# Performance work log

Measured on AMD Instinct MI355X. Metric: run time of the kernel, lower is better.

The kernel has to match this reference:

```python
import jax, jax.numpy as jnp
import numpy as np

N = 100000      # nodes
E = 3200000     # directed edges (avg degree 32)
D_IN = 128
H = 64
NEG_INF = -1e30


def setup_inputs() -> dict:
    key = jax.random.key(0)
    ks = jax.random.split(key, 16)
    s = 0.05
    return {
        "x": jax.random.normal(ks[0], (N, D_IN), jnp.float32),
        "edge_index": jax.random.randint(ks[1], (2, E), 0, N, jnp.int32),
        "ready": jax.random.randint(ks[2], (N, 1), 0, 2, jnp.int32),
        "W1": jax.random.normal(ks[3], (D_IN, H), jnp.float32) * s,
        "b1": jnp.zeros((H,), jnp.float32),
        "W2": jax.random.normal(ks[4], (H, H), jnp.float32) * s,
        "b2": jnp.zeros((H,), jnp.float32),
        "W3": jax.random.normal(ks[5], (H, H), jnp.float32) * s,
        "b3": jnp.zeros((H,), jnp.float32),
        "W4": jax.random.normal(ks[6], (H, H), jnp.float32) * s,
        "b4": jnp.zeros((H,), jnp.float32),
        "W5": jax.random.normal(ks[7], (H, 1), jnp.float32) * s,
        "b5": jnp.zeros((1,), jnp.float32),
        "Wdn": jax.random.normal(ks[8], (H, 1), jnp.float32) * s,
        "bdn": jnp.zeros((1,), jnp.float32),
        "Wv": jax.random.normal(ks[9], (H, 1), jnp.float32) * s,
        "bv": jnp.zeros((1,), jnp.float32),
    }


def _gcn_norm(edge_index):
    # add self-loops, then symmetric normalization.
    # flow='target_to_source': aggregate at row=edge_index[0], gather from col=edge_index[1],
    # degree computed on the row index (PyG gcn_norm with flow='target_to_source').
    loops = jnp.arange(N, dtype=edge_index.dtype)
    row = jnp.concatenate([edge_index[0], loops])
    col = jnp.concatenate([edge_index[1], loops])
    deg = jax.ops.segment_sum(jnp.ones(row.shape[0], jnp.float32), row, num_segments=N)
    dinv = jnp.where(deg > 0, jax.lax.rsqrt(deg), 0.0)
    norm = dinv[row] * dinv[col]
    return row, col, norm


def _gcn_conv(x, W, b, row, col, norm):
    h = x @ W                               # [N, d_out]
    m = norm[:, None] * h[col]              # gather messages from col
    out = jax.ops.segment_sum(m, row, num_segments=N)  # scatter-add at row
    return out + b


def reference(x, edge_index, ready, W1, b1, W2, b2, W3, b3, W4, b4, W5, b5, Wdn, bdn, Wv, bv):
    row, col, norm = _gcn_norm(edge_index)
    h = jax.nn.relu(_gcn_conv(x, W1, b1, row, col, norm))
    h = jax.nn.relu(_gcn_conv(h, W2, b2, row, col, norm))
    h = jax.nn.relu(_gcn_conv(h, W3, b3, row, col, norm))
    h = jax.nn.relu(_gcn_conv(h, W4, b4, row, col, norm))
    probs_nodes = _gcn_conv(h, W5, b5, row, col, norm)[:, 0]   # [N]
    x_mean = jnp.mean(h, axis=0)                               # [H]
    v = x_mean @ Wv + bv                                       # [1]
    prob_nothing = x_mean @ Wdn + bdn                          # [1]
    logits = jnp.concatenate([probs_nodes, prob_nothing])      # [N+1]
    mask = jnp.concatenate([ready[:, 0].astype(bool), jnp.array([True])])
    # masked softmax: softmax restricted to ready nodes + 'do nothing' slot;
    # non-ready positions get probability 0 (fixed-shape equivalent of torch's
    # boolean-index + softmax over the selected entries).
    probs = jax.nn.softmax(jnp.where(mask, logits, NEG_INF))
    return probs, v
```

## Files before the change

kernel.cpp:

```cpp
#include <hip/hip_runtime.h>
#include <hip/hip_bf16.h>
#include <hip/hip_fp16.h>


#define WAVE 64
#define BSHIFT 9
#define BROWS 512
#define ACHUNK 8192
#define CAP 17408

using half8  = __attribute__((ext_vector_type(8))) _Float16;
using float4v = __attribute__((ext_vector_type(4))) float;

__device__ __forceinline__ float waveSum(float v) {
  #pragma unroll
  for (int o = 32; o; o >>= 1) v += __shfl_xor(v, o);
  return v;
}
__device__ __forceinline__ float waveMax(float v) {
  #pragma unroll
  for (int o = 32; o; o >>= 1) v = fmaxf(v, __shfl_xor(v, o));
  return v;
}

__global__ void bucket_init(int* __restrict__ bucket_fill, int nbkt) {
  int b = blockIdx.x * blockDim.x + threadIdx.x;
  if (b < nbkt) bucket_fill[b] = b * CAP;
}

__global__ __launch_bounds__(256) void bin_edges(const int* __restrict__ ei,
                                                 int* __restrict__ bucket_fill,
                                                 int* __restrict__ eb, int E) {
  __shared__ int hist[256], basee[256], rank[256];
  int t = threadIdx.x;
  hist[t] = 0; rank[t] = 0;
  __syncthreads();
  int c0 = blockIdx.x * ACHUNK;
  #pragma unroll
  for (int k = 0; k < ACHUNK / 256; ++k) {
    int e = c0 + k * 256 + t;
    if (e < E) atomicAdd(&hist[ei[e] >> BSHIFT], 1);
  }
  __syncthreads();
  if (hist[t]) basee[t] = atomicAdd(&bucket_fill[t], hist[t]);
  __syncthreads();
  #pragma unroll
  for (int k = 0; k < ACHUNK / 256; ++k) {
    int e = c0 + k * 256 + t;
    if (e < E) {
      int r = ei[e], c = ei[E + e];
      int bb = r >> BSHIFT;
      int p = basee[bb] + atomicAdd(&rank[bb], 1);
      eb[p] = ((r & (BROWS - 1)) << 17) | c;
    }
  }
}

__global__ __launch_bounds__(256) void csr_bucket(const int* __restrict__ eb,
                                                  const int* __restrict__ bucket_fill,
                                                  int* __restrict__ row_s,
                                                  int* __restrict__ row_e,
                                                  float* __restrict__ dinv,
                                                  int* __restrict__ col_s, int N) {
  __shared__ int deg[BROWS], locp[BROWS], fill[BROWS], sh[256];
  int b = blockIdx.x;
  int base = b << BSHIFT;
  int R = min(BROWS, N - base);
  int t = threadIdx.x;
  deg[t] = 0; deg[t + 256] = 0;
  fill[t] = 0; fill[t + 256] = 0;
  __syncthreads();
  int E0 = b * CAP, E1 = bucket_fill[b];
  for (int e = E0 + t; e < E1; e += 256) atomicAdd(&deg[eb[e] >> 17], 1);
  __syncthreads();
  int d0 = deg[2 * t], d1 = deg[2 * t + 1];
  int s = d0 + d1;
  sh[t] = s;
  __syncthreads();
  for (int o = 1; o < 256; o <<= 1) {
    int x = (t >= o) ? sh[t - o] : 0;
    __syncthreads();
    sh[t] += x;
    __syncthreads();
  }
  int ex = sh[t] - s;
  locp[2 * t] = ex;
  locp[2 * t + 1] = ex + d0;
  __syncthreads();
  for (int i = t; i < R; i += 256) {
    int st = E0 + locp[i];
    row_s[base + i] = st;
    row_e[base + i] = st + deg[i];
    dinv[base + i] = rsqrtf((float)(deg[i] + 1));
  }
  for (int e = E0 + t; e < E1; e += 256) {
    int v = eb[e];
    int li = v >> 17;
    int p = E0 + locp[li] + atomicAdd(&fill[li], 1);
    col_s[p] = v & 0x1FFFF;
  }
}

template <int K, bool A32>
__global__ __launch_bounds__(256) void gemm_f16(const void* __restrict__ Ain,
                                                const float* __restrict__ Wg,
                                                const float* __restrict__ dinv,
                                                __half* __restrict__ Y, int N) {
  __shared__ _Float16 Wt[64][K + 8];
  int t = threadIdx.x;
  for (int idx = t; idx < K * 64; idx += 256) {
    int k = idx >> 6, n = idx & 63;
    Wt[n][k] = (_Float16)Wg[idx];
  }
  __syncthreads();
  int wave = t >> 6, lane = t & 63;
  int m = lane & 15, quad = lane >> 4;
  int r0 = blockIdx.x * 64 + wave * 16;
  float4v acc0 = {0.f, 0.f, 0.f, 0.f}, acc1 = {0.f, 0.f, 0.f, 0.f};
  float4v acc2 = {0.f, 0.f, 0.f, 0.f}, acc3 = {0.f, 0.f, 0.f, 0.f};
  int gr = r0 + m;
  bool valid = gr < N;
  int grs = valid ? gr : 0;
  const half8* arow = (const half8*)((const _Float16*)Ain + (size_t)grs * K);
  const float4* arow32 = (const float4*)((const float*)Ain + (size_t)grs * K);
  #pragma unroll
  for (int k0 = 0; k0 < K; k0 += 32) {
    half8 a = {};
    if (valid) {
      if (A32) {
        float4 f0 = arow32[(k0 >> 2) + quad * 2];
        float4 f1 = arow32[(k0 >> 2) + quad * 2 + 1];
        a = half8{(_Float16)f0.x, (_Float16)f0.y, (_Float16)f0.z, (_Float16)f0.w,
                  (_Float16)f1.x, (_Float16)f1.y, (_Float16)f1.z, (_Float16)f1.w};
      } else {
        a = arow[(k0 >> 3) + quad];
      }
    }
    half8 b0 = *(const half8*)&Wt[ 0 + m][k0 + quad * 8];
    half8 b1 = *(const half8*)&Wt[16 + m][k0 + quad * 8];
    half8 b2 = *(const half8*)&Wt[32 + m][k0 + quad * 8];
    half8 b3 = *(const half8*)&Wt[48 + m][k0 + quad * 8];
    acc0 = __builtin_amdgcn_mfma_f32_16x16x32_f16(a, b0, acc0, 0, 0, 0);
    acc1 = __builtin_amdgcn_mfma_f32_16x16x32_f16(a, b1, acc1, 0, 0, 0);
    acc2 = __builtin_amdgcn_mfma_f32_16x16x32_f16(a, b2, acc2, 0, 0, 0);
    acc3 = __builtin_amdgcn_mfma_f32_16x16x32_f16(a, b3, acc3, 0, 0, 0);
  }
  #pragma unroll
  for (int r = 0; r < 4; ++r) {
    int row = r0 + quad * 4 + r;
    if (row < N) {
      float dv = dinv[row];
      __half* dst = Y + (size_t)row * 64;
      dst[ 0 + m] = __float2half(acc0[r] * dv);
      dst[16 + m] = __float2half(acc1[r] * dv);
      dst[32 + m] = __float2half(acc2[r] * dv);
      dst[48 + m] = __float2half(acc3[r] * dv);
    }
  }
}

__device__ __forceinline__ float2 gather_row(const __half2* __restrict__ Y2,
                                             const int* __restrict__ col_s,
                                             int i, int p0, int p1,
                                             int lane, int half, int ch2) {
  float2 a0 = {0.f, 0.f}, a1 = {0.f, 0.f};
  if (half == 0) a0 = __half22float2(Y2[(size_t)i * 32 + ch2]);
  for (int base = p0; base < p1; base += 64) {
    int m = min(64, p1 - base);
    int c = 0;
    if (lane < m) c = col_s[base + lane];
    int j = 0;
    for (; j + 8 <= m; j += 8) {
      int c0 = __shfl(c, j + half);
      int c1 = __shfl(c, j + 2 + half);
      int c2 = __shfl(c, j + 4 + half);
      int c3 = __shfl(c, j + 6 + half);
      float2 y0 = __half22float2(Y2[(size_t)c0 * 32 + ch2]);
      float2 y1 = __half22float2(Y2[(size_t)c1 * 32 + ch2]);
      float2 y2 = __half22float2(Y2[(size_t)c2 * 32 + ch2]);
      float2 y3 = __half22float2(Y2[(size_t)c3 * 32 + ch2]);
      a0.x += y0.x + y1.x; a0.y += y0.y + y1.y;
      a1.x += y2.x + y3.x; a1.y += y2.y + y3.y;
    }
    for (; j < m; j += 2) {
      int idx = j + half;
      int cc = __shfl(c, idx);
      if (idx < m) {
        float2 y = __half22float2(Y2[(size_t)cc * 32 + ch2]);
        a0.x += y.x; a0.y += y.y;
      }
    }
  }
  float2 s;
  s.x = a0.x + a1.x;
  s.y = a0.y + a1.y;
  s.x += __shfl_xor(s.x, 32);
  s.y += __shfl_xor(s.y, 32);
  return s;
}

__global__ __launch_bounds__(256) void agg64(const __half* __restrict__ Ys,
                                             const int* __restrict__ col_s,
                                             const int* __restrict__ row_s,
                                             const int* __restrict__ row_e,
                                             const float* __restrict__ dinv,
                                             const float* __restrict__ bias,
                                             __half* __restrict__ Xh, int N) {
  int i = blockIdx.x * 4 + (threadIdx.x >> 6);
  if (i >= N) return;
  int lane = threadIdx.x & 63;
  int half = lane >> 5, ch2 = lane & 31;
  const __half2* Y2 = (const __half2*)Ys;
  float2 s = gather_row(Y2, col_s, i, row_s[i], row_e[i], lane, half, ch2);
  if (half == 0) {
    float2 b2 = ((const float2*)bias)[ch2];
    float di = dinv[i];
    float ox = fmaxf(di * s.x + b2.x, 0.f);
    float oy = fmaxf(di * s.y + b2.y, 0.f);
    ((__half2*)Xh)[(size_t)i * 32 + ch2] = __floats2half2_rn(ox, oy);
  }
}

__global__ __launch_bounds__(256) void agg64_final(const __half* __restrict__ Ys,
                                                   const int* __restrict__ col_s,
                                                   const int* __restrict__ row_s,
                                                   const int* __restrict__ row_e,
                                                   const float* __restrict__ dinv,
                                                   const float* __restrict__ b4,
                                                   const float* __restrict__ W5,
                                                   float* __restrict__ h5,
                                                   float* __restrict__ red_m, int N) {
  int wave = threadIdx.x >> 6, lane = threadIdx.x & 63;
  int half = lane >> 5, ch2 = lane & 31;
  const __half2* Y2 = (const __half2*)Ys;
  float2 w52 = ((const float2*)W5)[ch2];
  float2 b42 = ((const float2*)b4)[ch2];
  float2 msum = {0.f, 0.f};
  int base_i = blockIdx.x * 32 + wave * 8;
  for (int k = 0; k < 8; ++k) {
    int i = base_i + k;
    if (i >= N) break;
    float di = dinv[i];
    float2 s = gather_row(Y2, col_s, i, row_s[i], row_e[i], lane, half, ch2);
    float hx = fmaxf(di * s.x + b42.x, 0.f);
    float hy = fmaxf(di * s.y + b42.y, 0.f);
    msum.x += hx;
    msum.y += hy;
    float p = waveSum(hx * w52.x + hy * w52.y);
    if (lane == 0) h5[i] = di * p * 0.5f;
  }
  __shared__ float2 sh2[4][32];
  if (half == 0) sh2[wave][ch2] = msum;
  __syncthreads();
  if (threadIdx.x < 32) {
    int c = threadIdx.x;
    float tx = sh2[0][c].x + sh2[1][c].x + sh2[2][c].x + sh2[3][c].x;
    float ty = sh2[0][c].y + sh2[1][c].y + sh2[2][c].y + sh2[3][c].y;
    float* dst = &red_m[(blockIdx.x & 7) * 64];
    atomicAdd(&dst[2 * c], tx);
    atomicAdd(&dst[2 * c + 1], ty);
  }
}

__global__ __launch_bounds__(256) void agg_scalar(const float* __restrict__ h5,
                                                  const int* __restrict__ col_s,
                                                  const int* __restrict__ row_s,
                                                  const int* __restrict__ row_e,
                                                  const float* __restrict__ dinv,
                                                  const float* __restrict__ b5,
                                                  float* __restrict__ out, int N) {
  int i = blockIdx.x * 4 + (threadIdx.x >> 6);
  if (i >= N) return;
  int lane = threadIdx.x & 63;
  int p0 = row_s[i], p1 = row_e[i];
  float acc = 0.f;
  for (int p = p0 + lane; p < p1; p += 64) acc += h5[col_s[p]];
  acc = waveSum(acc);
  if (lane == 0) out[i] = dinv[i] * (acc + h5[i]) + b5[0];
}

__global__ void heads(const float* __restrict__ red_m, const float* __restrict__ Wv,
                      const float* __restrict__ bv, const float* __restrict__ Wdn,
                      const float* __restrict__ bdn, float* __restrict__ out, int N) {
  int lane = threadIdx.x;
  float s = 0.f;
  #pragma unroll
  for (int r = 0; r < 8; ++r) s += red_m[r * 64 + lane];
  float xm = s / (float)N;
  float pv = waveSum(xm * Wv[lane]);
  float pd = waveSum(xm * Wdn[lane]);
  if (lane == 0) {
    out[N] = pd + bdn[0];
    out[N + 1] = pv + bv[0];
  }
}

__global__ void smax_pass1(const float* __restrict__ out, const int* __restrict__ ready,
                           float* __restrict__ bm, float* __restrict__ bs, int N) {
  int i = blockIdx.x * 256 + threadIdx.x;
  bool valid = false;
  float l = -3e38f;
  if (i < N) { if (ready[i]) { valid = true; l = out[i]; } }
  else if (i == N) { valid = true; l = out[N]; }
  float m = waveMax(l);
  __shared__ float shm[4], shs[4];
  int wv = threadIdx.x >> 6;
  if ((threadIdx.x & 63) == 0) shm[wv] = m;
  __syncthreads();
  float bmax = fmaxf(fmaxf(shm[0], shm[1]), fmaxf(shm[2], shm[3]));
  float e = valid ? expf(l - bmax) : 0.f;
  float s = waveSum(e);
  if ((threadIdx.x & 63) == 0) shs[wv] = s;
  __syncthreads();
  if (threadIdx.x == 0) {
    bm[blockIdx.x] = bmax;
    bs[blockIdx.x] = shs[0] + shs[1] + shs[2] + shs[3];
  }
}

__global__ void smax_comb(const float* __restrict__ bm, const float* __restrict__ bs,
                          float* __restrict__ red, int NB) {
  int t = threadIdx.x;
  float m = -3e38f;
  for (int b = t; b < NB; b += 256) m = fmaxf(m, bm[b]);
  m = waveMax(m);
  __shared__ float shm[4], shs[4];
  if ((t & 63) == 0) shm[t >> 6] = m;
  __syncthreads();
  float M = fmaxf(fmaxf(shm[0], shm[1]), fmaxf(shm[2], shm[3]));
  float s = 0.f;
  for (int b = t; b < NB; b += 256) s += bs[b] * expf(bm[b] - M);
  s = waveSum(s);
  if ((t & 63) == 0) shs[t >> 6] = s;
  __syncthreads();
  if (t == 0) { red[0] = M; red[1] = shs[0] + shs[1] + shs[2] + shs[3]; }
}

__global__ void smax_write(float* __restrict__ out, const int* __restrict__ ready,
                           const float* __restrict__ red, int N) {
  float M = red[0];
  float S = red[1];
  int i = blockIdx.x * blockDim.x + threadIdx.x;
  if (i < N) {
    out[i] = ready[i] ? (expf(out[i] - M) / S) : 0.f;
  } else if (i == N) {
    out[N] = expf(out[N] - M) / S;
  }
}

extern "C" void kernel_launch(void* const* d_in, const int* in_sizes, int n_in,
                              void* d_out, int out_size, void* d_ws, size_t ws_size,
                              hipStream_t stream) {
  const float* x    = (const float*)d_in[0];
  const int*   ei   = (const int*)d_in[1];
  const int*   ready= (const int*)d_in[2];
  const float* W1   = (const float*)d_in[3];
  const float* b1   = (const float*)d_in[4];
  const float* W2   = (const float*)d_in[5];
  const float* b2   = (const float*)d_in[6];
  const float* W3   = (const float*)d_in[7];
  const float* b3   = (const float*)d_in[8];
  const float* W4   = (const float*)d_in[9];
  const float* b4   = (const float*)d_in[10];
  const float* W5   = (const float*)d_in[11];
  const float* b5   = (const float*)d_in[12];
  const float* Wdn  = (const float*)d_in[13];
  const float* bdn  = (const float*)d_in[14];
  const float* Wv   = (const float*)d_in[15];
  const float* bv   = (const float*)d_in[16];
  float* out = (float*)d_out;

  int N = in_sizes[2];
  int E = in_sizes[1] / 2;
  int nbkt = (N + BROWS - 1) >> BSHIFT;

  char* base = (char*)d_ws;
  size_t off = 0;
  auto allocB = [&](size_t bytes) -> void* {
    void* p = base + off;
    off += ((bytes + 255) / 256) * 256;
    return p;
  };
  size_t capBytes = (size_t)nbkt * CAP * 4;
  float*    dinv       = (float*)allocB((size_t)N * 4);
  int*      row_s      = (int*)allocB((size_t)N * 4);
  int*      row_e      = (int*)allocB((size_t)N * 4);
  int*      bucket_fill= (int*)allocB(256 * 4);
  int*      col_s      = (int*)allocB(capBytes);
  float*    h5         = (float*)allocB((size_t)N * 4);
  float*    red        = (float*)allocB(128 * 4);
  float*    red_m      = (float*)allocB(512 * 4);
  float*    bm         = (float*)allocB(512 * 4);
  float*    bs         = (float*)allocB(512 * 4);
  size_t ybBytes = (size_t)N * 64 * 2;
  __half*   Yb         = (__half*)allocB(capBytes > ybBytes ? capBytes : ybBytes);
  __half*   Xh         = (__half*)allocB((size_t)N * 64 * 2);
  int*      eb         = (int*)Yb;
  (void)ws_size; (void)n_in; (void)out_size;

  int gN1 = (N + 1 + 255) / 256;
  int gW = (N + 3) / 4;
  int gF = (N + 31) / 32;
  int gA = (E + ACHUNK - 1) / ACHUNK;
  int gG = (N + 63) / 64;

  hipMemsetAsync(red_m, 0, 512 * 4, stream);
  bucket_init<<<1, 256, 0, stream>>>(bucket_fill, nbkt);
  bin_edges<<<gA, 256, 0, stream>>>(ei, bucket_fill, eb, E);
  csr_bucket<<<nbkt, 256, 0, stream>>>(eb, bucket_fill, row_s, row_e, dinv,
                                       col_s, N);

  gemm_f16<128, true><<<gG, 256, 0, stream>>>(x, W1, dinv, Yb, N);
  agg64<<<gW, 256, 0, stream>>>(Yb, col_s, row_s, row_e, dinv, b1, Xh, N);
  gemm_f16<64, false><<<gG, 256, 0, stream>>>(Xh, W2, dinv, Yb, N);
  agg64<<<gW, 256, 0, stream>>>(Yb, col_s, row_s, row_e, dinv, b2, Xh, N);
  gemm_f16<64, false><<<gG, 256, 0, stream>>>(Xh, W3, dinv, Yb, N);
  agg64<<<gW, 256, 0, stream>>>(Yb, col_s, row_s, row_e, dinv, b3, Xh, N);
  gemm_f16<64, false><<<gG, 256, 0, stream>>>(Xh, W4, dinv, Yb, N);
  agg64_final<<<gF, 256, 0, stream>>>(Yb, col_s, row_s, row_e, dinv, b4, W5,
                                      h5, red_m, N);

  agg_scalar<<<gW, 256, 0, stream>>>(h5, col_s, row_s, row_e, dinv, b5, out, N);
  heads<<<1, 64, 0, stream>>>(red_m, Wv, bv, Wdn, bdn, out, N);

  smax_pass1<<<gN1, 256, 0, stream>>>(out, ready, bm, bs, N);
  smax_comb<<<1, 256, 0, stream>>>(bm, bs, red, gN1);
  smax_write<<<gN1, 256, 0, stream>>>(out, ready, red, N);
}
```

Baseline: 531.2 us.

## Column-block CSR edges and gather many rows per wave slab by slab

The CSR build now sorts each row's edges into eight column slabs of 16384 nodes and stores a per-row array of slab start offsets in place of row_s and row_e. The 64-channel aggregation kernels give each wave 25 consecutive rows and walk the column slabs in order, so that feature-row gathers from different rows fall into one limited region of Y at a time. The aim is better L2 reuse of the gathered features. In exchange, each wave handles many short per-slab segments, which lowers wave count and parallelism, and the per-row index array grows from two ints to eight.

```diff
diff --git a/kernel.cpp b/kernel.cpp
--- a/kernel.cpp
+++ b/kernel.cpp
@@ -8,6 +8,9 @@
 #define BROWS 512
 #define ACHUNK 8192
 #define CAP 17408
+#define NBLK 8
+#define BLKSHIFT 14
+#define NPW 25
 
 using half8  = __attribute__((ext_vector_type(8))) _Float16;
 using float4v = __attribute__((ext_vector_type(4))) float;
@@ -58,23 +61,29 @@
 
 __global__ __launch_bounds__(256) void csr_bucket(const int* __restrict__ eb,
                                                   const int* __restrict__ bucket_fill,
-                                                  int* __restrict__ row_s,
-                                                  int* __restrict__ row_e,
+                                                  int* __restrict__ row_bp,
                                                   float* __restrict__ dinv,
                                                   int* __restrict__ col_s, int N) {
-  __shared__ int deg[BROWS], locp[BROWS], fill[BROWS], sh[256];
+  __shared__ int deg[BROWS * NBLK];
+  __shared__ int fill[BROWS * NBLK];
+  __shared__ int sh[256];
   int b = blockIdx.x;
   int base = b << BSHIFT;
   int R = min(BROWS, N - base);
   int t = threadIdx.x;
-  deg[t] = 0; deg[t + 256] = 0;
-  fill[t] = 0; fill[t + 256] = 0;
+  for (int q = t; q < BROWS * NBLK; q += 256) { deg[q] = 0; fill[q] = 0; }
   __syncthreads();
   int E0 = b * CAP, E1 = bucket_fill[b];
-  for (int e = E0 + t; e < E1; e += 256) atomicAdd(&deg[eb[e] >> 17], 1);
-  __syncthreads();
-  int d0 = deg[2 * t], d1 = deg[2 * t + 1];
-  int s = d0 + d1;
+  int tot = E1 - E0;
+  for (int e = E0 + t; e < E1; e += 256) {
+    int v = eb[e];
+    atomicAdd(&deg[(v >> 17) * NBLK + ((v & 0x1FFFF) >> BLKSHIFT)], 1);
+  }
+  __syncthreads();
+  int loc[16];
+  int s = 0;
+  #pragma unroll
+  for (int q = 0; q < 16; ++q) { loc[q] = s; s += deg[t * 16 + q]; }
   sh[t] = s;
   __syncthreads();
   for (int o = 1; o < 256; o <<= 1) {
@@ -84,20 +93,23 @@
     __syncthreads();
   }
   int ex = sh[t] - s;
-  locp[2 * t] = ex;
-  locp[2 * t + 1] = ex + d0;
+  #pragma unroll
+  for (int q = 0; q < 16; ++q) deg[t * 16 + q] = ex + loc[q];
   __syncthreads();
   for (int i = t; i < R; i += 256) {
-    int st = E0 + locp[i];
-    row_s[base + i] = st;
-    row_e[base + i] = st + deg[i];
-    dinv[base + i] = rsqrtf((float)(deg[i] + 1));
+    int st = deg[i * NBLK];
+    int en = (i == BROWS - 1) ? tot : deg[(i + 1) * NBLK];
+    dinv[base + i] = rsqrtf((float)(en - st + 1));
+    #pragma unroll
+    for (int q = 0; q < NBLK; ++q)
+      row_bp[(size_t)(base + i) * NBLK + q] = E0 + deg[i * NBLK + q];
   }
   for (int e = E0 + t; e < E1; e += 256) {
     int v = eb[e];
-    int li = v >> 17;
-    int p = E0 + locp[li] + atomicAdd(&fill[li], 1);
-    col_s[p] = v & 0x1FFFF;
+    int c = v & 0x1FFFF;
+    int cell = (v >> 17) * NBLK + (c >> BLKSHIFT);
+    int p = E0 + deg[cell] + atomicAdd(&fill[cell], 1);
+    col_s[p] = c;
   }
 }
 
@@ -159,95 +171,133 @@
   }
 }
 
-__device__ __forceinline__ float2 gather_row(const __half2* __restrict__ Y2,
-                                             const int* __restrict__ col_s,
-                                             int i, int p0, int p1,
-                                             int lane, int half, int ch2) {
-  float2 a0 = {0.f, 0.f}, a1 = {0.f, 0.f};
-  if (half == 0) a0 = __half22float2(Y2[(size_t)i * 32 + ch2]);
-  for (int base = p0; base < p1; base += 64) {
-    int m = min(64, p1 - base);
-    int c = 0;
-    if (lane < m) c = col_s[base + lane];
-    int j = 0;
-    for (; j + 8 <= m; j += 8) {
-      int c0 = __shfl(c, j + half);
-      int c1 = __shfl(c, j + 2 + half);
-      int c2 = __shfl(c, j + 4 + half);
-      int c3 = __shfl(c, j + 6 + half);
-      float2 y0 = __half22float2(Y2[(size_t)c0 * 32 + ch2]);
-      float2 y1 = __half22float2(Y2[(size_t)c1 * 32 + ch2]);
-      float2 y2 = __half22float2(Y2[(size_t)c2 * 32 + ch2]);
-      float2 y3 = __half22float2(Y2[(size_t)c3 * 32 + ch2]);
-      a0.x += y0.x + y1.x; a0.y += y0.y + y1.y;
-      a1.x += y2.x + y3.x; a1.y += y2.y + y3.y;
-    }
-    for (; j < m; j += 2) {
-      int idx = j + half;
-      int cc = __shfl(c, idx);
-      if (idx < m) {
-        float2 y = __half22float2(Y2[(size_t)cc * 32 + ch2]);
-        a0.x += y.x; a0.y += y.y;
-      }
-    }
-  }
-  float2 s;
-  s.x = a0.x + a1.x;
-  s.y = a0.y + a1.y;
-  s.x += __shfl_xor(s.x, 32);
-  s.y += __shfl_xor(s.y, 32);
-  return s;
-}
-
-__global__ __launch_bounds__(256) void agg64(const __half* __restrict__ Ys,
-                                             const int* __restrict__ col_s,
-                                             const int* __restrict__ row_s,
-                                             const int* __restrict__ row_e,
-                                             const float* __restrict__ dinv,
-                                             const float* __restrict__ bias,
-                                             __half* __restrict__ Xh, int N) {
-  int i = blockIdx.x * 4 + (threadIdx.x >> 6);
-  if (i >= N) return;
+#define GATHER_PASSES(acc, i0, N, Y2, col_s, row_bp, lane, half, ch2)          \
+  _Pragma("unroll 1")                                                          \
+  for (int b = 0; b < 7; ++b) {                                                \
+    _Pragma("unroll")                                                          \
+    for (int k = 0; k < NPW; ++k) {                                            \
+      int i = (i0) + k;                                                        \
+      if (i >= (N)) continue;                                                  \
+      int p0 = row_bp[(size_t)i * NBLK + b];                                   \
+      int p1 = row_bp[(size_t)i * NBLK + b + 1];                               \
+      for (int bs = p0; bs < p1; bs += 64) {                                   \
+        int mm = min(64, p1 - bs);                                             \
+        int cv = (lane < mm) ? col_s[bs + lane] : 0;                           \
+        int j = 0;                                                             \
+        for (; j + 4 <= mm; j += 4) {                                          \
+          int c0 = __shfl(cv, j + half);                                       \
+          int c1 = __shfl(cv, j + 2 + half);                                   \
+          float2 y0 = __half22float2(Y2[(size_t)c0 * 32 + ch2]);               \
+          float2 y1 = __half22float2(Y2[(size_t)c1 * 32 + ch2]);               \
+          acc[k].x += y0.x + y1.x; acc[k].y += y0.y + y1.y;                    \
+        }                                                                      \
+        for (; j < mm; j += 2) {                                               \
+          int idx = j + half;                                                  \
+          int cc = __shfl(cv, idx);                                            \
+          if (idx < mm) {                                                      \
+            float2 y = __half22float2(Y2[(size_t)cc * 32 + ch2]);              \
+            acc[k].x += y.x; acc[k].y += y.y;                                  \
+          }                                                                    \
+        }                                                                      \
+      }                                                                        \
+    }                                                                          \
+  }
+
+__global__ __launch_bounds__(256, 4) void agg64(const __half* __restrict__ Ys,
+                                                const int* __restrict__ col_s,
+                                                const int* __restrict__ row_bp,
+                                                const float* __restrict__ dinv,
+                                                const float* __restrict__ bias,
+                                                __half* __restrict__ Xh, int N) {
+  int wv = blockIdx.x * 4 + (threadIdx.x >> 6);
+  int i0 = wv * NPW;
+  if (i0 >= N) return;
   int lane = threadIdx.x & 63;
   int half = lane >> 5, ch2 = lane & 31;
   const __half2* Y2 = (const __half2*)Ys;
-  float2 s = gather_row(Y2, col_s, i, row_s[i], row_e[i], lane, half, ch2);
+  float2 acc[NPW];
+  #pragma unroll
+  for (int k = 0; k < NPW; ++k) acc[k] = float2{0.f, 0.f};
+  if (half == 0) {
+    #pragma unroll
+    for (int k = 0; k < NPW; ++k) {
+      int i = i0 + k;
+      if (i < N) {
+        float2 y = __half22float2(Y2[(size_t)i * 32 + ch2]);
+        acc[k].x += y.x; acc[k].y += y.y;
+      }
+    }
+  }
+  GATHER_PASSES(acc, i0, N, Y2, col_s, row_bp, lane, half, ch2)
+  #pragma unroll
+  for (int k = 0; k < NPW; ++k) {
+    acc[k].x += __shfl_xor(acc[k].x, 32);
+    acc[k].y += __shfl_xor(acc[k].y, 32);
+  }
   if (half == 0) {
     float2 b2 = ((const float2*)bias)[ch2];
-    float di = dinv[i];
-    float ox = fmaxf(di * s.x + b2.x, 0.f);
-    float oy = fmaxf(di * s.y + b2.y, 0.f);
-    ((__half2*)Xh)[(size_t)i * 32 + ch2] = __floats2half2_rn(ox, oy);
-  }
-}
-
-__global__ __launch_bounds__(256) void agg64_final(const __half* __restrict__ Ys,
-                                                   const int* __restrict__ col_s,
-                                                   const int* __restrict__ row_s,
-                                                   const int* __restrict__ row_e,
-                                                   const float* __restrict__ dinv,
-                                                   const float* __restrict__ b4,
-                                                   const float* __restrict__ W5,
-                                                   float* __restrict__ h5,
-                                                   float* __restrict__ red_m, int N) {
+    #pragma unroll
+    for (int k = 0; k < NPW; ++k) {
+      int i = i0 + k;
+      if (i < N) {
+        float di = dinv[i];
+        ((__half2*)Xh)[(size_t)i * 32 + ch2] =
+            __floats2half2_rn(fmaxf(di * acc[k].x + b2.x, 0.f),
+                              fmaxf(di * acc[k].y + b2.y, 0.f));
+      }
+    }
+  }
+}
+
+__global__ __launch_bounds__(256, 4) void agg64_final(const __half* __restrict__ Ys,
+                                                      const int* __restrict__ col_s,
+                                                      const int* __restrict__ row_bp,
+                                                      const float* __restrict__ dinv,
+                                                      const float* __restrict__ b4,
+                                                      const float* __restrict__ W5,
+                                                      float* __restrict__ h5,
+                                                      float* __restrict__ red_m, int N) {
   int wave = threadIdx.x >> 6, lane = threadIdx.x & 63;
   int half = lane >> 5, ch2 = lane & 31;
+  int wv = blockIdx.x * 4 + wave;
+  int i0 = wv * NPW;
   const __half2* Y2 = (const __half2*)Ys;
   float2 w52 = ((const float2*)W5)[ch2];
   float2 b42 = ((const float2*)b4)[ch2];
   float2 msum = {0.f, 0.f};
-  int base_i = blockIdx.x * 32 + wave * 8;
-  for (int k = 0; k < 8; ++k) {
-    int i = base_i + k;
-    if (i >= N) break;
-    float di = dinv[i];
-    float2 s = gather_row(Y2, col_s, i, row_s[i], row_e[i], lane, half, ch2);
-    float hx = fmaxf(di * s.x + b42.x, 0.f);
-    float hy = fmaxf(di * s.y + b42.y, 0.f);
-    msum.x += hx;
-    msum.y += hy;
-    float p = waveSum(hx * w52.x + hy * w52.y);
-    if (lane == 0) h5[i] = di * p * 0.5f;
+  if (i0 < N) {
+    float2 acc[NPW];
+    #pragma unroll
+    for (int k = 0; k < NPW; ++k) acc[k] = float2{0.f, 0.f};
+    if (half == 0) {
+      #pragma unroll
+      for (int k = 0; k < NPW; ++k) {
+        int i = i0 + k;
+        if (i < N) {
+          float2 y = __half22float2(Y2[(size_t)i * 32 + ch2]);
+          acc[k].x += y.x; acc[k].y += y.y;
+        }
+      }
+    }
+    GATHER_PASSES(acc, i0, N, Y2, col_s, row_bp, lane, half, ch2)
+    #pragma unroll
+    for (int k = 0; k < NPW; ++k) {
+      acc[k].x += __shfl_xor(acc[k].x, 32);
+      acc[k].y += __shfl_xor(acc[k].y, 32);
+    }
+    #pragma unroll
+    for (int k = 0; k < NPW; ++k) {
+      int i = i0 + k;
+      if (i < N) {
+        float di = dinv[i];
+        float hx = fmaxf(di * acc[k].x + b42.x, 0.f);
+        float hy = fmaxf(di * acc[k].y + b42.y, 0.f);
+        msum.x += hx;
+        msum.y += hy;
+        float p = waveSum(hx * w52.x + hy * w52.y);
+        if (lane == 0) h5[i] = di * p * 0.5f;
+      }
+    }
   }
   __shared__ float2 sh2[4][32];
   if (half == 0) sh2[wave][ch2] = msum;
@@ -264,15 +314,15 @@
 
 __global__ __launch_bounds__(256) void agg_scalar(const float* __restrict__ h5,
                                                   const int* __restrict__ col_s,
-                                                  const int* __restrict__ row_s,
-                                                  const int* __restrict__ row_e,
+                                                  const int* __restrict__ row_bp,
                                                   const float* __restrict__ dinv,
                                                   const float* __restrict__ b5,
                                                   float* __restrict__ out, int N) {
   int i = blockIdx.x * 4 + (threadIdx.x >> 6);
   if (i >= N) return;
   int lane = threadIdx.x & 63;
-  int p0 = row_s[i], p1 = row_e[i];
+  int p0 = row_bp[(size_t)i * NBLK];
+  int p1 = row_bp[(size_t)i * NBLK + 7];
   float acc = 0.f;
   for (int p = p0 + lane; p < p1; p += 64) acc += h5[col_s[p]];
   acc = waveSum(acc);
@@ -383,8 +433,7 @@
   };
   size_t capBytes = (size_t)nbkt * CAP * 4;
   float*    dinv       = (float*)allocB((size_t)N * 4);
-  int*      row_s      = (int*)allocB((size_t)N * 4);
-  int*      row_e      = (int*)allocB((size_t)N * 4);
+  int*      row_bp     = (int*)allocB((size_t)N * NBLK * 4);
   int*      bucket_fill= (int*)allocB(256 * 4);
   int*      col_s      = (int*)allocB(capBytes);
   float*    h5         = (float*)allocB((size_t)N * 4);
@@ -400,27 +449,27 @@
 
   int gN1 = (N + 1 + 255) / 256;
   int gW = (N + 3) / 4;
-  int gF = (N + 31) / 32;
+  int nwaves = (N + NPW - 1) / NPW;
+  int gAgg = (nwaves + 3) / 4;
   int gA = (E + ACHUNK - 1) / ACHUNK;
   int gG = (N + 63) / 64;
 
   hipMemsetAsync(red_m, 0, 512 * 4, stream);
   bucket_init<<<1, 256, 0, stream>>>(bucket_fill, nbkt);
   bin_edges<<<gA, 256, 0, stream>>>(ei, bucket_fill, eb, E);
-  csr_bucket<<<nbkt, 256, 0, stream>>>(eb, bucket_fill, row_s, row_e, dinv,
-                                       col_s, N);
+  csr_bucket<<<nbkt, 256, 0, stream>>>(eb, bucket_fill, row_bp, dinv, col_s, N);
 
   gemm_f16<128, true><<<gG, 256, 0, stream>>>(x, W1, dinv, Yb, N);
-  agg64<<<gW, 256, 0, stream>>>(Yb, col_s, row_s, row_e, dinv, b1, Xh, N);
+  agg64<<<gAgg, 256, 0, stream>>>(Yb, col_s, row_bp, dinv, b1, Xh, N);
   gemm_f16<64, false><<<gG, 256, 0, stream>>>(Xh, W2, dinv, Yb, N);
-  agg64<<<gW, 256, 0, stream>>>(Yb, col_s, row_s, row_e, dinv, b2, Xh, N);
+  agg64<<<gAgg, 256, 0, stream>>>(Yb, col_s, row_bp, dinv, b2, Xh, N);
   gemm_f16<64, false><<<gG, 256, 0, stream>>>(Xh, W3, dinv, Yb, N);
-  agg64<<<gW, 256, 0, stream>>>(Yb, col_s, row_s, row_e, dinv, b3, Xh, N);
+  agg64<<<gAgg, 256, 0, stream>>>(Yb, col_s, row_bp, dinv, b3, Xh, N);
   gemm_f16<64, false><<<gG, 256, 0, stream>>>(Xh, W4, dinv, Yb, N);
-  agg64_final<<<gF, 256, 0, stream>>>(Yb, col_s, row_s, row_e, dinv, b4, W5,
-                                      h5, red_m, N);
-
-  agg_scalar<<<gW, 256, 0, stream>>>(h5, col_s, row_s, row_e, dinv, b5, out, N);
+  agg64_final<<<gAgg, 256, 0, stream>>>(Yb, col_s, row_bp, dinv, b4, W5,
+                                        h5, red_m, N);
+
+  agg_scalar<<<gW, 256, 0, stream>>>(h5, col_s, row_bp, dinv, b5, out, N);
   heads<<<1, 64, 0, stream>>>(red_m, Wv, bv, Wdn, bdn, out, N);
 
   smax_pass1<<<gN1, 256, 0, stream>>>(out, ready, bm, bs, N);
```

After: 1.227 ms. 2.31x slower.
